# Kernel optimization log

Hardware: AMD Instinct MI355X
Metric: run time of the kernel (lower is better)

The kernel has to match this reference:

```python
import jax, jax.numpy as jnp
import numpy as np

N = 100000; E = 1600000; D_IN = 9; HID = 16; HEADS = 8; D = HID * HEADS; G = 1000
NEG_SLOPE = 0.2; LN_EPS = 1e-5


def _gat_conv(x, src, dst, W, a_src, a_dst, b, heads, ch):
    # PyG GATConv (eval mode, self-loops already appended to src/dst)
    h = (x @ W).reshape(-1, heads, ch)                   # [N,H,C]
    al_s = (h * a_src).sum(-1)                           # [N,H]
    al_d = (h * a_dst).sum(-1)                           # [N,H]
    e = al_s[src] + al_d[dst]                            # [Et,H]
    e = jnp.where(e > 0, e, NEG_SLOPE * e)               # LeakyReLU(0.2)
    m = jax.ops.segment_max(e, dst, num_segments=N)      # per-dst softmax
    alpha = jnp.exp(e - m[dst])
    denom = jax.ops.segment_sum(alpha, dst, num_segments=N)
    alpha = alpha / (denom[dst] + 1e-16)
    out = jax.ops.segment_sum(h[src] * alpha[:, :, None], dst, num_segments=N)
    return out.reshape(-1, heads * ch) + b


def _ln_graph(x, g, b):
    # PyG LayerNorm, mode='graph', batch=None: normalize over all nodes+channels
    mu = x.mean()
    var = jnp.mean((x - mu) ** 2)
    return (x - mu) / jnp.sqrt(var + LN_EPS) * g + b


def setup_inputs() -> dict:
    key = jax.random.key(0)
    ks = jax.random.split(key, 20)
    s = 0.1
    p = lambda i, shape: jax.random.normal(ks[i], shape, jnp.float32) * s
    return {
        "x": jax.random.normal(ks[0], (N, D_IN), jnp.float32),
        "edge_index": jax.random.randint(ks[1], (2, E), 0, N),
        "batch": jnp.sort(jax.random.randint(ks[2], (N,), 0, G)),
        "W1": p(3, (D_IN, D)), "a_src1": p(4, (HEADS, HID)), "a_dst1": p(5, (HEADS, HID)), "b1": jnp.zeros((D,), jnp.float32),
        "W2": p(6, (D, D)), "a_src2": p(7, (1, D)), "a_dst2": p(8, (1, D)), "b2": jnp.zeros((D,), jnp.float32),
        "fc1_w": p(9, (D, D)), "fc1_b": jnp.zeros((D,), jnp.float32),
        "fc2_w": p(10, (D, D)), "fc2_b": jnp.zeros((D,), jnp.float32),
        "fc3_w": p(11, (D, D)), "fc3_b": jnp.zeros((D,), jnp.float32),
        "fc4_w": p(12, (D, D)), "fc4_b": jnp.zeros((D,), jnp.float32),
        "g1": jnp.ones((D,), jnp.float32), "beta1": jnp.zeros((D,), jnp.float32),
        "g2": jnp.ones((D,), jnp.float32), "beta2": jnp.zeros((D,), jnp.float32),
        "fcf_w": p(13, (D, 1)), "fcf_b": jnp.zeros((1,), jnp.float32),
    }


def reference(x, edge_index, batch, W1, a_src1, a_dst1, b1, W2, a_src2, a_dst2, b2,
              fc1_w, fc1_b, fc2_w, fc2_b, fc3_w, fc3_b, fc4_w, fc4_b,
              g1, beta1, g2, beta2, fcf_w, fcf_b):
    loops = jnp.arange(N)
    src = jnp.concatenate([edge_index[0], loops])
    dst = jnp.concatenate([edge_index[1], loops])
    h = jax.nn.relu(_gat_conv(x, src, dst, W1, a_src1, a_dst1, b1, HEADS, HID))
    hc = h
    h = jax.nn.relu(h @ fc1_w + fc1_b)
    h = jax.nn.relu(h @ fc2_w + fc2_b + hc)
    h = _ln_graph(h, g1, beta1)
    hc = h
    h = _gat_conv(h, src, dst, W2, a_src2, a_dst2, b2, 1, D)
    h = jax.nn.relu(h @ fc3_w + fc3_b)
    h = h @ fc4_w + fc4_b + hc
    h = _ln_graph(h, g2, beta2)
    h = h @ fcf_w + fcf_b                                # [N,1]
    sums = jax.ops.segment_sum(h, batch, num_segments=G)
    cnt = jax.ops.segment_sum(jnp.ones((N,), h.dtype), batch, num_segments=G)
    return sums / jnp.maximum(cnt, 1.0)[:, None]          # global_mean_pool -> [G,1]
```

## Files before the change

### kernel.cpp

```cpp
#include <hip/hip_runtime.h>
#include <cstdint>

#define NN 100000
#define NE 1600000
#define DI 9
#define DD 128
#define NH 8
#define NG 1000

#define NBK 3125
#define NBLK 256
#define EPB (NE/NBLK)

typedef unsigned int uint;
typedef __attribute__((ext_vector_type(8))) short bf16x8;
typedef __attribute__((ext_vector_type(4))) float f32x4;

__device__ __forceinline__ float leaky(float x){ return x > 0.f ? x : 0.2f*x; }
__device__ __forceinline__ uint f2bf(float f){
  uint u = __float_as_uint(f);
  return (u + 0x7fffu + ((u>>16)&1u)) >> 16;
}
__device__ __forceinline__ float bflo(uint p){ return __uint_as_float(p << 16); }
__device__ __forceinline__ float bfhi(uint p){ return __uint_as_float(p & 0xffff0000u); }
__device__ __forceinline__ uint packbf(float a, float b){ return f2bf(a) | (f2bf(b)<<16); }

union U16 { uint4 u; bf16x8 v; };
__device__ __forceinline__ bf16x8 ld8(const uint* p){ U16 t; t.u = *(const uint4*)p; return t.v; }

__global__ __launch_bounds__(512) void k_hist(const int* __restrict__ dst, int* __restrict__ hist){
  __shared__ int h[NBK];
  for (int i = threadIdx.x; i < NBK; i += 512) h[i] = 0;
  __syncthreads();
  int blk = blockIdx.x;
  int beg = blk*EPB, end = beg + EPB;
  for (int i = beg + threadIdx.x; i < end; i += 512)
    atomicAdd(&h[dst[i] >> 5], 1);
  __syncthreads();
  for (int b = threadIdx.x; b < NBK; b += 512) hist[b*NBLK + blk] = h[b];
}

__global__ __launch_bounds__(256) void k_bsum(int* __restrict__ hist, int* __restrict__ bsum){
  int b = blockIdx.x*256 + threadIdx.x;
  if (b >= NBK) return;
  int run = 0;
  #pragma unroll 4
  for (int k = 0; k < NBLK; ++k){
    int t = hist[b*NBLK + k];
    hist[b*NBLK + k] = run;
    run += t;
  }
  bsum[b] = run;
}

__global__ __launch_bounds__(1024) void k_bscan(const int* __restrict__ bsum, int* __restrict__ bbase){
  __shared__ int sh[1024];
  __shared__ int carry;
  if (threadIdx.x == 0) carry = 0;
  __syncthreads();
  for (int c0 = 0; c0 < NBK; c0 += 1024){
    int i = c0 + threadIdx.x;
    int v = (i < NBK) ? bsum[i] : 0;
    sh[threadIdx.x] = v;
    __syncthreads();
    for (int off = 1; off < 1024; off <<= 1){
      int t = (threadIdx.x >= off) ? sh[threadIdx.x-off] : 0;
      __syncthreads();
      sh[threadIdx.x] += t;
      __syncthreads();
    }
    if (i < NBK) bbase[i] = carry + sh[threadIdx.x] - v;
    __syncthreads();
    if (threadIdx.x == 0) carry += sh[1023];
    __syncthreads();
  }
}

__global__ __launch_bounds__(512) void k_part(const int* __restrict__ src, const int* __restrict__ dst,
    const int* __restrict__ hist, const int* __restrict__ bbase, uint* __restrict__ ebuf){
  __shared__ int cur[NBK];
  int blk = blockIdx.x;
  for (int b = threadIdx.x; b < NBK; b += 512)
    cur[b] = hist[b*NBLK + blk] + bbase[b];
  __syncthreads();
  int beg = blk*EPB, end = beg + EPB;
  for (int i = beg + threadIdx.x; i < end; i += 512){
    int d = dst[i], s = src[i];
    int b = d >> 5;
    int p = atomicAdd(&cur[b], 1);
    ebuf[p] = (uint)s | ((uint)(d & 31) << 26);
  }
}

__global__ __launch_bounds__(64) void k_fin(const uint* __restrict__ ebuf, const int* __restrict__ bbase,
    const int* __restrict__ bsum, int* __restrict__ rowptr, int* __restrict__ col){
  __shared__ int cnt32[32];
  __shared__ int exc[32];
  int b = blockIdx.x;
  int lane = threadIdx.x;
  if (lane < 32) cnt32[lane] = 0;
  __syncthreads();
  int base = bbase[b], n = bsum[b];
  for (int i = lane; i < n; i += 64)
    atomicAdd(&cnt32[ebuf[base+i] >> 26], 1);
  __syncthreads();
  if (lane == 0){
    int run = 0;
    for (int d = 0; d < 32; ++d){
      int t = cnt32[d];
      exc[d] = run;
      rowptr[b*32 + d] = base + run;
      run += t;
    }
  }
  __syncthreads();
  if (lane < 32) cnt32[lane] = exc[lane];
  __syncthreads();
  for (int i = lane; i < n; i += 64){
    uint e = ebuf[base+i];
    int d = e >> 26;
    int r = atomicAdd(&cnt32[d], 1);
    col[base + r] = (int)(e & 0x03ffffffu);
  }
  if (b == 0 && lane == 0) rowptr[NN] = NE;
}

__global__ __launch_bounds__(64) void k_wconv(const float* __restrict__ W, uint* __restrict__ WT){
  int n = blockIdx.x;
  int t = threadIdx.x;
  float w0 = W[(2*t)*DD + n];
  float w1 = W[(2*t+1)*DD + n];
  WT[n*64 + t] = packbf(w0, w1);
}

__global__ __launch_bounds__(128) void k_lin1(const float* __restrict__ x, const float* __restrict__ W1,
    const float* __restrict__ as1, const float* __restrict__ ad1,
    uint* __restrict__ t1b, float* __restrict__ al_s, float* __restrict__ al_d){
  int n = blockIdx.x;
  int c = threadIdx.x;
  const float* xr = x + n*DI;
  float t = 0.f;
  #pragma unroll
  for (int k = 0; k < DI; ++k) t = fmaf(xr[k], W1[k*DD+c], t);
  uint mybf = f2bf(t);
  uint pbf  = (uint)__shfl_xor((int)mybf, 1, 64);
  if (!(c & 1)) t1b[(size_t)n*64 + (c>>1)] = mybf | (pbf<<16);
  float vs = t * as1[c];
  float vd = t * ad1[c];
  #pragma unroll
  for (int m = 8; m >= 1; m >>= 1){ vs += __shfl_xor(vs, m, 16); vd += __shfl_xor(vd, m, 16); }
  if ((c & 15) == 0){
    al_s[n*NH + (c>>4)] = vs;
    al_d[n*NH + (c>>4)] = vd;
  }
}

__global__ __launch_bounds__(256) void k_gat1(const uint* __restrict__ t1b,
    const float* __restrict__ al_s, const float* __restrict__ al_d,
    const int* __restrict__ rowptr, const int* __restrict__ col,
    const float* __restrict__ b1, uint* __restrict__ outb){
  int n = blockIdx.x*4 + (threadIdx.x >> 6);
  if (n >= NN) return;
  uint lane = threadIdx.x & 63;
  uint h = lane >> 3;
  float ald = al_d[(uint)n*NH + h];
  float a0  = __expf(leaky(al_s[(uint)n*NH + h] + ald));
  uint  ps  = t1b[(uint)n*64u + lane];
  float den = a0;
  float s0 = a0*bflo(ps), s1 = a0*bfhi(ps);
  int beg = rowptr[n], end = rowptr[n+1];
  int e = beg;
  for (; e + 8 <= end; e += 8){
    uint c0 = (uint)col[e],   c1 = (uint)col[e+1], c2 = (uint)col[e+2], c3 = (uint)col[e+3];
    uint c4 = (uint)col[e+4], c5 = (uint)col[e+5], c6 = (uint)col[e+6], c7 = (uint)col[e+7];
    float l0 = al_s[c0*8u + h], l1 = al_s[c1*8u + h], l2 = al_s[c2*8u + h], l3 = al_s[c3*8u + h];
    float l4 = al_s[c4*8u + h], l5 = al_s[c5*8u + h], l6 = al_s[c6*8u + h], l7 = al_s[c7*8u + h];
    uint p0 = t1b[c0*64u + lane], p1 = t1b[c1*64u + lane];
    uint p2 = t1b[c2*64u + lane], p3 = t1b[c3*64u + lane];
    uint p4 = t1b[c4*64u + lane], p5 = t1b[c5*64u + lane];
    uint p6 = t1b[c6*64u + lane], p7 = t1b[c7*64u + lane];
    float a0_ = __expf(leaky(l0 + ald)), a1_ = __expf(leaky(l1 + ald));
    float a2_ = __expf(leaky(l2 + ald)), a3_ = __expf(leaky(l3 + ald));
    float a4_ = __expf(leaky(l4 + ald)), a5_ = __expf(leaky(l5 + ald));
    float a6_ = __expf(leaky(l6 + ald)), a7_ = __expf(leaky(l7 + ald));
    den += a0_ + a1_ + a2_ + a3_ + a4_ + a5_ + a6_ + a7_;
    s0 = fmaf(a0_, bflo(p0), s0); s1 = fmaf(a0_, bfhi(p0), s1);
    s0 = fmaf(a1_, bflo(p1), s0); s1 = fmaf(a1_, bfhi(p1), s1);
    s0 = fmaf(a2_, bflo(p2), s0); s1 = fmaf(a2_, bfhi(p2), s1);
    s0 = fmaf(a3_, bflo(p3), s0); s1 = fmaf(a3_, bfhi(p3), s1);
    s0 = fmaf(a4_, bflo(p4), s0); s1 = fmaf(a4_, bfhi(p4), s1);
    s0 = fmaf(a5_, bflo(p5), s0); s1 = fmaf(a5_, bfhi(p5), s1);
    s0 = fmaf(a6_, bflo(p6), s0); s1 = fmaf(a6_, bfhi(p6), s1);
    s0 = fmaf(a7_, bflo(p7), s0); s1 = fmaf(a7_, bfhi(p7), s1);
  }
  for (; e < end; ++e){
    uint c = (uint)col[e];
    float a = __expf(leaky(al_s[c*8u + h] + ald));
    uint p = t1b[c*64u + lane];
    den += a;
    s0 = fmaf(a, bflo(p), s0); s1 = fmaf(a, bfhi(p), s1);
  }
  float inv = 1.f/(den + 1e-16f);
  float2 bb = ((const float2*)b1)[lane];
  outb[(uint)n*64u + lane] = packbf(fmaxf(s0*inv + bb.x, 0.f), fmaxf(s1*inv + bb.y, 0.f));
}

__global__ __launch_bounds__(256) void k_gat2(const uint* __restrict__ t2b,
    const float* __restrict__ al_s, const float* __restrict__ al_d,
    const int* __restrict__ rowptr, const int* __restrict__ col,
    const float* __restrict__ b2, uint* __restrict__ outb){
  int n = blockIdx.x*4 + (threadIdx.x >> 6);
  if (n >= NN) return;
  uint lane = threadIdx.x & 63;
  float ald = al_d[n];
  float a0  = __expf(leaky(al_s[n] + ald));
  uint  ps  = t2b[(uint)n*64u + lane];
  float den = a0;
  float s0 = a0*bflo(ps), s1 = a0*bfhi(ps);
  int beg = rowptr[n], end = rowptr[n+1];
  int e = beg;
  for (; e + 8 <= end; e += 8){
    uint c0 = (uint)col[e],   c1 = (uint)col[e+1], c2 = (uint)col[e+2], c3 = (uint)col[e+3];
    uint c4 = (uint)col[e+4], c5 = (uint)col[e+5], c6 = (uint)col[e+6], c7 = (uint)col[e+7];
    float l0 = al_s[c0], l1 = al_s[c1], l2 = al_s[c2], l3 = al_s[c3];
    float l4 = al_s[c4], l5 = al_s[c5], l6 = al_s[c6], l7 = al_s[c7];
    uint p0 = t2b[c0*64u + lane], p1 = t2b[c1*64u + lane];
    uint p2 = t2b[c2*64u + lane], p3 = t2b[c3*64u + lane];
    uint p4 = t2b[c4*64u + lane], p5 = t2b[c5*64u + lane];
    uint p6 = t2b[c6*64u + lane], p7 = t2b[c7*64u + lane];
    float a0_ = __expf(leaky(l0 + ald)), a1_ = __expf(leaky(l1 + ald));
    float a2_ = __expf(leaky(l2 + ald)), a3_ = __expf(leaky(l3 + ald));
    float a4_ = __expf(leaky(l4 + ald)), a5_ = __expf(leaky(l5 + ald));
    float a6_ = __expf(leaky(l6 + ald)), a7_ = __expf(leaky(l7 + ald));
    den += a0_ + a1_ + a2_ + a3_ + a4_ + a5_ + a6_ + a7_;
    s0 = fmaf(a0_, bflo(p0), s0); s1 = fmaf(a0_, bfhi(p0), s1);
    s0 = fmaf(a1_, bflo(p1), s0); s1 = fmaf(a1_, bfhi(p1), s1);
    s0 = fmaf(a2_, bflo(p2), s0); s1 = fmaf(a2_, bfhi(p2), s1);
    s0 = fmaf(a3_, bflo(p3), s0); s1 = fmaf(a3_, bfhi(p3), s1);
    s0 = fmaf(a4_, bflo(p4), s0); s1 = fmaf(a4_, bfhi(p4), s1);
    s0 = fmaf(a5_, bflo(p5), s0); s1 = fmaf(a5_, bfhi(p5), s1);
    s0 = fmaf(a6_, bflo(p6), s0); s1 = fmaf(a6_, bfhi(p6), s1);
    s0 = fmaf(a7_, bflo(p7), s0); s1 = fmaf(a7_, bfhi(p7), s1);
  }
  for (; e < end; ++e){
    uint c = (uint)col[e];
    float a = __expf(leaky(al_s[c] + ald));
    uint p = t2b[c*64u + lane];
    den += a;
    s0 = fmaf(a, bflo(p), s0); s1 = fmaf(a, bfhi(p), s1);
  }
  float inv = 1.f/(den + 1e-16f);
  float2 bb = ((const float2*)b2)[lane];
  outb[(uint)n*64u + lane] = packbf(s0*inv + bb.x, s1*inv + bb.y);
}

template<bool RELU, bool BIAS, bool RES, bool LNRED, bool AL2>
__global__ __launch_bounds__(256) void k_mfma(const uint* __restrict__ Xb, const uint* __restrict__ WTb,
    const float* __restrict__ bias, const uint* __restrict__ resb, uint* __restrict__ outb,
    float* __restrict__ pbuf, const float* __restrict__ avs, const float* __restrict__ avd,
    float* __restrict__ o_als, float* __restrict__ o_ald, int nrows){
  int lane = threadIdx.x & 63;
  int wid  = threadIdx.x >> 6;
  int m0 = blockIdx.x*128 + wid*32;
  int lr = lane & 15, hi4 = lane >> 4;
  f32x4 acc[2][8];
  #pragma unroll
  for (int a = 0; a < 2; ++a)
    #pragma unroll
    for (int c = 0; c < 8; ++c) acc[a][c] = (f32x4){0.f,0.f,0.f,0.f};
  int ra0 = m0 + lr;      if (ra0 > NN-1) ra0 = NN-1;
  int ra1 = m0 + 16 + lr; if (ra1 > NN-1) ra1 = NN-1;
  #pragma unroll
  for (int kk = 0; kk < 4; ++kk){
    int ko = kk*16 + hi4*4;
    bf16x8 a0 = ld8(Xb + (size_t)ra0*64 + ko);
    bf16x8 a1 = ld8(Xb + (size_t)ra1*64 + ko);
    #pragma unroll
    for (int c = 0; c < 8; ++c){
      bf16x8 b = ld8(WTb + (size_t)(c*16 + lr)*64 + ko);
      acc[0][c] = __builtin_amdgcn_mfma_f32_16x16x32_bf16(a0, b, acc[0][c], 0, 0, 0);
      acc[1][c] = __builtin_amdgcn_mfma_f32_16x16x32_bf16(a1, b, acc[1][c], 0, 0, 0);
    }
  }
  if (AL2){
    #pragma unroll
    for (int rg = 0; rg < 2; ++rg){
      #pragma unroll
      for (int r = 0; r < 4; ++r){
        float vs = 0.f, vd = 0.f;
        #pragma unroll
        for (int c = 0; c < 8; ++c){
          float v = acc[rg][c][r];
          vs = fmaf(v, avs[c*16 + lr], vs);
          vd = fmaf(v, avd[c*16 + lr], vd);
        }
        #pragma unroll
        for (int m = 8; m >= 1; m >>= 1){ vs += __shfl_xor(vs, m, 64); vd += __shfl_xor(vd, m, 64); }
        int row = m0 + rg*16 + hi4*4 + r;
        if (lr == 0 && row < nrows){ o_als[row] = vs; o_ald[row] = vd; }
      }
    }
  }
  bool evn = !(lane & 1);
  int cph = lr >> 1;
  float lns = 0.f, lnss = 0.f;
  #pragma unroll
  for (int rg = 0; rg < 2; ++rg){
    #pragma unroll
    for (int c = 0; c < 8; ++c){
      int cp = c*8 + cph;
      #pragma unroll
      for (int r = 0; r < 4; ++r){
        float v0 = acc[rg][c][r];
        float v1 = __shfl_xor(v0, 1, 64);
        int row = m0 + rg*16 + hi4*4 + r;
        if (evn && row < nrows){
          if (BIAS){ float2 bb = ((const float2*)bias)[cp]; v0 += bb.x; v1 += bb.y; }
          if (RES){ uint rr = resb[(size_t)row*64 + cp]; v0 += bflo(rr); v1 += bfhi(rr); }
          if (RELU){ v0 = fmaxf(v0, 0.f); v1 = fmaxf(v1, 0.f); }
          outb[(size_t)row*64 + cp] = packbf(v0, v1);
          if (LNRED){ lns += v0 + v1; lnss += v0*v0 + v1*v1; }
        }
      }
    }
  }
  if (LNRED){
    #pragma unroll
    for (int m = 32; m >= 1; m >>= 1){ lns += __shfl_xor(lns, m, 64); lnss += __shfl_xor(lnss, m, 64); }
    __shared__ float shred[8];
    if (lane == 0){ shred[wid*2] = lns; shred[wid*2+1] = lnss; }
    __syncthreads();
    if (threadIdx.x == 0){
      float S = 0.f, SS = 0.f;
      for (int w = 0; w < 4; ++w){ S += shred[2*w]; SS += shred[2*w+1]; }
      pbuf[blockIdx.x*2] = S; pbuf[blockIdx.x*2+1] = SS;
    }
  }
}

__global__ __launch_bounds__(256) void k_ln_stats(const float* __restrict__ pbuf, float* __restrict__ stats, int nb){
  float s = 0.f, ss = 0.f;
  for (int i = threadIdx.x; i < nb; i += 256){ s += pbuf[2*i]; ss += pbuf[2*i+1]; }
  #pragma unroll
  for (int m = 32; m >= 1; m >>= 1){ s += __shfl_xor(s, m, 64); ss += __shfl_xor(ss, m, 64); }
  __shared__ float sh[8];
  int wid = threadIdx.x >> 6, lane = threadIdx.x & 63;
  if (lane == 0){ sh[wid*2] = s; sh[wid*2+1] = ss; }
  __syncthreads();
  if (threadIdx.x == 0){
    float S = 0.f, SS = 0.f;
    for (int w = 0; w < 4; ++w){ S += sh[2*w]; SS += sh[2*w+1]; }
    const float inv = 1.f/((float)NN*(float)DD);
    float mu = S*inv;
    float var = SS*inv - mu*mu;
    stats[0] = mu;
    stats[1] = rsqrtf(var + 1e-5f);
  }
}

__global__ __launch_bounds__(256) void k_ln_apply_bf(uint* __restrict__ xb, const float* __restrict__ g,
    const float* __restrict__ be, const float* __restrict__ stats){
  const int n4 = NN*16;
  float mu = stats[0], rs = stats[1];
  uint4* x4 = (uint4*)xb;
  const float2* g2 = (const float2*)g;
  const float2* b2 = (const float2*)be;
  for (int i = blockIdx.x*256 + threadIdx.x; i < n4; i += gridDim.x*256){
    int cb = (i & 15)*4;
    uint4 u = x4[i];
    float2 ga = g2[cb],   gb = g2[cb+1], gc = g2[cb+2], gd = g2[cb+3];
    float2 ba = b2[cb],   bb = b2[cb+1], bc = b2[cb+2], bd = b2[cb+3];
    u.x = packbf((bflo(u.x)-mu)*rs*ga.x + ba.x, (bfhi(u.x)-mu)*rs*ga.y + ba.y);
    u.y = packbf((bflo(u.y)-mu)*rs*gb.x + bb.x, (bfhi(u.y)-mu)*rs*gb.y + bb.y);
    u.z = packbf((bflo(u.z)-mu)*rs*gc.x + bc.x, (bfhi(u.z)-mu)*rs*gc.y + bc.y);
    u.w = packbf((bflo(u.w)-mu)*rs*gd.x + bd.x, (bfhi(u.w)-mu)*rs*gd.y + bd.y);
    x4[i] = u;
  }
}

__global__ __launch_bounds__(256) void k_fdot_ln(const uint* __restrict__ xb, const float* __restrict__ g,
    const float* __restrict__ be, const float* __restrict__ stats,
    const float* __restrict__ fw, const float* __restrict__ fb, float* __restrict__ val){
  int n = blockIdx.x*4 + (threadIdx.x >> 6);
  if (n >= NN) return;
  int lane = threadIdx.x & 63;
  float mu = stats[0], rs = stats[1];
  uint p = xb[(size_t)n*64 + lane];
  float2 gg = ((const float2*)g)[lane];
  float2 bb = ((const float2*)be)[lane];
  float2 ww = ((const float2*)fw)[lane];
  float v = ((bflo(p)-mu)*rs*gg.x + bb.x)*ww.x + ((bfhi(p)-mu)*rs*gg.y + bb.y)*ww.y;
  #pragma unroll
  for (int m = 32; m >= 1; m >>= 1) v += __shfl_xor(v, m, 64);
  if (lane == 0) val[n] = v + fb[0];
}

__global__ __launch_bounds__(64) void k_pool(const float* __restrict__ val, const int* __restrict__ batch,
                                             float* __restrict__ out){
  int g = blockIdx.x;
  int lane = threadIdx.x;
  int lo = 0, hi = NN;
  while (lo < hi){ int mid = (lo+hi)>>1; if (batch[mid] < g) lo = mid+1; else hi = mid; }
  int start = lo;
  hi = NN;
  while (lo < hi){ int mid = (lo+hi)>>1; if (batch[mid] < g+1) lo = mid+1; else hi = mid; }
  int end = lo;
  float s = 0.f;
  for (int i = start + lane; i < end; i += 64) s += val[i];
  #pragma unroll
  for (int m = 32; m >= 1; m >>= 1) s += __shfl_xor(s, m, 64);
  if (lane == 0) out[g] = s / fmaxf((float)(end - start), 1.f);
}

extern "C" void kernel_launch(void* const* d_in, const int* in_sizes, int n_in,
                              void* d_out, int out_size, void* d_ws, size_t ws_size,
                              hipStream_t stream){
  const float* x   = (const float*)d_in[0];
  const int*   ei  = (const int*)d_in[1];
  const int* batch = (const int*)d_in[2];
  const float* W1  = (const float*)d_in[3];
  const float* as1 = (const float*)d_in[4];
  const float* ad1 = (const float*)d_in[5];
  const float* b1  = (const float*)d_in[6];
  const float* W2  = (const float*)d_in[7];
  const float* as2 = (const float*)d_in[8];
  const float* ad2 = (const float*)d_in[9];
  const float* b2  = (const float*)d_in[10];
  const float* fc1w= (const float*)d_in[11];
  const float* fc1b= (const float*)d_in[12];
  const float* fc2w= (const float*)d_in[13];
  const float* fc2b= (const float*)d_in[14];
  const float* fc3w= (const float*)d_in[15];
  const float* fc3b= (const float*)d_in[16];
  const float* fc4w= (const float*)d_in[17];
  const float* fc4b= (const float*)d_in[18];
  const float* g1  = (const float*)d_in[19];
  const float* be1 = (const float*)d_in[20];
  const float* g2  = (const float*)d_in[21];
  const float* be2 = (const float*)d_in[22];
  const float* fcw = (const float*)d_in[23];
  const float* fcb = (const float*)d_in[24];
  float* out = (float*)d_out;
  (void)in_sizes; (void)n_in; (void)out_size; (void)ws_size;

  char* ws = (char*)d_ws;
  size_t off = 0;
  auto alloc = [&](size_t bytes)->void*{
    void* p = ws + off;
    off += (bytes + 255) & ~(size_t)255;
    return p;
  };
  float* A    = (float*)alloc((size_t)NN*DD*4);
  float* B    = (float*)alloc((size_t)NN*DD*4);
  float* C    = (float*)alloc((size_t)NN*DD*4);
  float* als1 = (float*)alloc((size_t)NN*NH*4);
  float* ald1 = (float*)alloc((size_t)NN*NH*4);
  float* als2 = (float*)alloc((size_t)NN*4);
  float* ald2 = (float*)alloc((size_t)NN*4);
  float* escr = (float*)alloc((size_t)NE*4);
  int*   rowptr = (int*)alloc((size_t)(NN+1)*4);
  int*   col    = (int*)alloc((size_t)NE*4);
  int*   bsum   = (int*)alloc((size_t)NBK*4);
  int*   bbase  = (int*)alloc((size_t)NBK*4);
  float* pbuf   = (float*)alloc(1024*2*4);
  float* stats  = (float*)alloc(2*4);
  float* val    = (float*)alloc((size_t)NN*4);
  uint* wt_fc1  = (uint*)alloc((size_t)DD*64*4);
  uint* wt_fc2  = (uint*)alloc((size_t)DD*64*4);
  uint* wt_w2   = (uint*)alloc((size_t)DD*64*4);
  uint* wt_fc3  = (uint*)alloc((size_t)DD*64*4);
  uint* wt_fc4  = (uint*)alloc((size_t)DD*64*4);

  uint*  Ab     = (uint*)A;
  uint*  Bb     = (uint*)B;
  uint*  Cb     = (uint*)C;
  int*   hist   = (int*)A;
  uint*  ebuf   = (uint*)escr;

  const int* esrc = ei;
  const int* edst = ei + NE;

  k_hist <<<NBLK, 512, 0, stream>>>(edst, hist);
  k_bsum <<<(NBK+255)/256, 256, 0, stream>>>(hist, bsum);
  k_bscan<<<1, 1024, 0, stream>>>(bsum, bbase);
  k_part <<<NBLK, 512, 0, stream>>>(esrc, edst, hist, bbase, ebuf);
  k_fin  <<<NBK, 64, 0, stream>>>(ebuf, bbase, bsum, rowptr, col);

  k_wconv<<<DD, 64, 0, stream>>>(fc1w, wt_fc1);
  k_wconv<<<DD, 64, 0, stream>>>(fc2w, wt_fc2);
  k_wconv<<<DD, 64, 0, stream>>>(W2,   wt_w2);
  k_wconv<<<DD, 64, 0, stream>>>(fc3w, wt_fc3);
  k_wconv<<<DD, 64, 0, stream>>>(fc4w, wt_fc4);

  const int WB = (NN + 3)/4;
  const int GB = (NN + 127)/128;

  k_lin1<<<NN, 128, 0, stream>>>(x, W1, as1, ad1, Ab, als1, ald1);
  k_gat1<<<WB, 256, 0, stream>>>(Ab, als1, ald1, rowptr, col, b1, Bb);

  k_mfma<true,  true, false, false, false><<<GB, 256, 0, stream>>>(Bb, wt_fc1, fc1b, nullptr, Ab, nullptr, nullptr, nullptr, nullptr, nullptr, NN);
  k_mfma<true,  true, true,  true,  false><<<GB, 256, 0, stream>>>(Ab, wt_fc2, fc2b, Bb,      Cb, pbuf,    nullptr, nullptr, nullptr, nullptr, NN);

  k_ln_stats<<<1, 256, 0, stream>>>(pbuf, stats, GB);
  k_ln_apply_bf<<<1024, 256, 0, stream>>>(Cb, g1, be1, stats);

  k_mfma<false, false, false, false, true ><<<GB, 256, 0, stream>>>(Cb, wt_w2, nullptr, nullptr, Ab, nullptr, as2, ad2, als2, ald2, NN);
  k_gat2<<<WB, 256, 0, stream>>>(Ab, als2, ald2, rowptr, col, b2, Bb);

  k_mfma<true,  true, false, false, false><<<GB, 256, 0, stream>>>(Bb, wt_fc3, fc3b, nullptr, Ab, nullptr, nullptr, nullptr, nullptr, nullptr, NN);
  k_mfma<false, true, true,  true,  false><<<GB, 256, 0, stream>>>(Ab, wt_fc4, fc4b, Cb,      Bb, pbuf,    nullptr, nullptr, nullptr, nullptr, NN);

  k_ln_stats<<<1, 256, 0, stream>>>(pbuf, stats, GB);
  k_fdot_ln<<<WB, 256, 0, stream>>>(Bb, g2, be2, stats, fcw, fcb, val);
  k_pool<<<NG, 64, 0, stream>>>(val, batch, out);
}
```

Before: 506.6 us.

## Fuse paired MLP GEMMs through LDS, batch weight conversion, transpose histogram layout

Adds k_mfma2, which runs two back-to-back 128x128 bf16 MFMA GEMMs in one kernel. The ReLU'd intermediate stays in shared memory, so it is never written to and reread from global memory. The kernel also applies the residual, the optional ReLU and the LayerNorm partial sums. The five weight-conversion launches become one kernel that picks its matrix from the block index. The bucket histogram is stored block-major, so the per-bucket prefix loop in k_bsum reads memory coalesced across threads. The fused kernel uses more shared memory and registers per block, which may reduce occupancy.

```diff
diff --git a/kernel.cpp b/kernel.cpp
--- a/kernel.cpp
+++ b/kernel.cpp
@@ -27,6 +27,7 @@
 
 union U16 { uint4 u; bf16x8 v; };
 __device__ __forceinline__ bf16x8 ld8(const uint* p){ U16 t; t.u = *(const uint4*)p; return t.v; }
+__device__ __forceinline__ bf16x8 ld8lds(const uint* p){ U16 t; t.u = *(const uint4*)p; return t.v; }
 
 __global__ __launch_bounds__(512) void k_hist(const int* __restrict__ dst, int* __restrict__ hist){
   __shared__ int h[NBK];
@@ -37,17 +38,16 @@
   for (int i = beg + threadIdx.x; i < end; i += 512)
     atomicAdd(&h[dst[i] >> 5], 1);
   __syncthreads();
-  for (int b = threadIdx.x; b < NBK; b += 512) hist[b*NBLK + blk] = h[b];
+  for (int b = threadIdx.x; b < NBK; b += 512) hist[(size_t)blk*NBK + b] = h[b];
 }
 
 __global__ __launch_bounds__(256) void k_bsum(int* __restrict__ hist, int* __restrict__ bsum){
   int b = blockIdx.x*256 + threadIdx.x;
   if (b >= NBK) return;
   int run = 0;
-  #pragma unroll 4
   for (int k = 0; k < NBLK; ++k){
-    int t = hist[b*NBLK + k];
-    hist[b*NBLK + k] = run;
+    int t = hist[(size_t)k*NBK + b];
+    hist[(size_t)k*NBK + b] = run;
     run += t;
   }
   bsum[b] = run;
@@ -81,7 +81,7 @@
   __shared__ int cur[NBK];
   int blk = blockIdx.x;
   for (int b = threadIdx.x; b < NBK; b += 512)
-    cur[b] = hist[b*NBLK + blk] + bbase[b];
+    cur[b] = hist[(size_t)blk*NBK + b] + bbase[b];
   __syncthreads();
   int beg = blk*EPB, end = beg + EPB;
   for (int i = beg + threadIdx.x; i < end; i += 512){
@@ -125,12 +125,18 @@
   if (b == 0 && lane == 0) rowptr[NN] = NE;
 }
 
-__global__ __launch_bounds__(64) void k_wconv(const float* __restrict__ W, uint* __restrict__ WT){
-  int n = blockIdx.x;
+__global__ __launch_bounds__(64) void k_wconv5(const float* __restrict__ w0, const float* __restrict__ w1,
+    const float* __restrict__ w2, const float* __restrict__ w3, const float* __restrict__ w4,
+    uint* __restrict__ o0, uint* __restrict__ o1, uint* __restrict__ o2,
+    uint* __restrict__ o3, uint* __restrict__ o4){
+  int which = blockIdx.x >> 7;
+  int n = blockIdx.x & 127;
   int t = threadIdx.x;
-  float w0 = W[(2*t)*DD + n];
-  float w1 = W[(2*t+1)*DD + n];
-  WT[n*64 + t] = packbf(w0, w1);
+  const float* W = (which==0)?w0:(which==1)?w1:(which==2)?w2:(which==3)?w3:w4;
+  uint* WT = (which==0)?o0:(which==1)?o1:(which==2)?o2:(which==3)?o3:o4;
+  float a = W[(2*t)*DD + n];
+  float b = W[(2*t+1)*DD + n];
+  WT[n*64 + t] = packbf(a, b);
 }
 
 __global__ __launch_bounds__(128) void k_lin1(const float* __restrict__ x, const float* __restrict__ W1,
@@ -338,6 +344,108 @@
   }
 }
 
+template<bool RELU2>
+__global__ __launch_bounds__(256) void k_mfma2(const uint* __restrict__ Xb,
+    const uint* __restrict__ WT1b, const float* __restrict__ bias1,
+    const uint* __restrict__ WT2b, const float* __restrict__ bias2,
+    const uint* __restrict__ resb, uint* __restrict__ outb,
+    float* __restrict__ pbuf, int nrows){
+  __shared__ uint Y1[128][68];
+  int lane = threadIdx.x & 63;
+  int wid  = threadIdx.x >> 6;
+  int m0 = blockIdx.x*128 + wid*32;
+  int lr = lane & 15, hi4 = lane >> 4;
+  bool evn = !(lane & 1);
+  int cph = lr >> 1;
+  f32x4 acc[2][8];
+  #pragma unroll
+  for (int a = 0; a < 2; ++a)
+    #pragma unroll
+    for (int c = 0; c < 8; ++c) acc[a][c] = (f32x4){0.f,0.f,0.f,0.f};
+  int ra0 = m0 + lr;      if (ra0 > NN-1) ra0 = NN-1;
+  int ra1 = m0 + 16 + lr; if (ra1 > NN-1) ra1 = NN-1;
+  #pragma unroll
+  for (int kk = 0; kk < 4; ++kk){
+    int ko = kk*16 + hi4*4;
+    bf16x8 a0 = ld8(Xb + (size_t)ra0*64 + ko);
+    bf16x8 a1 = ld8(Xb + (size_t)ra1*64 + ko);
+    #pragma unroll
+    for (int c = 0; c < 8; ++c){
+      bf16x8 b = ld8(WT1b + (size_t)(c*16 + lr)*64 + ko);
+      acc[0][c] = __builtin_amdgcn_mfma_f32_16x16x32_bf16(a0, b, acc[0][c], 0, 0, 0);
+      acc[1][c] = __builtin_amdgcn_mfma_f32_16x16x32_bf16(a1, b, acc[1][c], 0, 0, 0);
+    }
+  }
+  #pragma unroll
+  for (int rg = 0; rg < 2; ++rg){
+    #pragma unroll
+    for (int c = 0; c < 8; ++c){
+      int cp = c*8 + cph;
+      #pragma unroll
+      for (int r = 0; r < 4; ++r){
+        float v0 = acc[rg][c][r];
+        float v1 = __shfl_xor(v0, 1, 64);
+        if (evn){
+          float2 bb = ((const float2*)bias1)[cp];
+          v0 = fmaxf(v0 + bb.x, 0.f); v1 = fmaxf(v1 + bb.y, 0.f);
+          int lrow = wid*32 + rg*16 + hi4*4 + r;
+          Y1[lrow][cp] = packbf(v0, v1);
+        }
+      }
+    }
+  }
+  __syncthreads();
+  #pragma unroll
+  for (int a = 0; a < 2; ++a)
+    #pragma unroll
+    for (int c = 0; c < 8; ++c) acc[a][c] = (f32x4){0.f,0.f,0.f,0.f};
+  #pragma unroll
+  for (int kk = 0; kk < 4; ++kk){
+    int ko = kk*16 + hi4*4;
+    bf16x8 a0 = ld8lds(&Y1[wid*32 + lr][ko]);
+    bf16x8 a1 = ld8lds(&Y1[wid*32 + 16 + lr][ko]);
+    #pragma unroll
+    for (int c = 0; c < 8; ++c){
+      bf16x8 b = ld8(WT2b + (size_t)(c*16 + lr)*64 + ko);
+      acc[0][c] = __builtin_amdgcn_mfma_f32_16x16x32_bf16(a0, b, acc[0][c], 0, 0, 0);
+      acc[1][c] = __builtin_amdgcn_mfma_f32_16x16x32_bf16(a1, b, acc[1][c], 0, 0, 0);
+    }
+  }
+  float lns = 0.f, lnss = 0.f;
+  #pragma unroll
+  for (int rg = 0; rg < 2; ++rg){
+    #pragma unroll
+    for (int c = 0; c < 8; ++c){
+      int cp = c*8 + cph;
+      #pragma unroll
+      for (int r = 0; r < 4; ++r){
+        float v0 = acc[rg][c][r];
+        float v1 = __shfl_xor(v0, 1, 64);
+        int row = m0 + rg*16 + hi4*4 + r;
+        if (evn && row < nrows){
+          float2 bb = ((const float2*)bias2)[cp];
+          v0 += bb.x; v1 += bb.y;
+          uint rr = resb[(size_t)row*64 + cp];
+          v0 += bflo(rr); v1 += bfhi(rr);
+          if (RELU2){ v0 = fmaxf(v0, 0.f); v1 = fmaxf(v1, 0.f); }
+          outb[(size_t)row*64 + cp] = packbf(v0, v1);
+          lns += v0 + v1; lnss += v0*v0 + v1*v1;
+        }
+      }
+    }
+  }
+  #pragma unroll
+  for (int m = 32; m >= 1; m >>= 1){ lns += __shfl_xor(lns, m, 64); lnss += __shfl_xor(lnss, m, 64); }
+  __shared__ float shred[8];
+  if (lane == 0){ shred[wid*2] = lns; shred[wid*2+1] = lnss; }
+  __syncthreads();
+  if (threadIdx.x == 0){
+    float S = 0.f, SS = 0.f;
+    for (int w = 0; w < 4; ++w){ S += shred[2*w]; SS += shred[2*w+1]; }
+    pbuf[blockIdx.x*2] = S; pbuf[blockIdx.x*2+1] = SS;
+  }
+}
+
 __global__ __launch_bounds__(256) void k_ln_stats(const float* __restrict__ pbuf, float* __restrict__ stats, int nb){
   float s = 0.f, ss = 0.f;
   for (int i = threadIdx.x; i < nb; i += 256){ s += pbuf[2*i]; ss += pbuf[2*i+1]; }
@@ -486,11 +594,8 @@
   k_part <<<NBLK, 512, 0, stream>>>(esrc, edst, hist, bbase, ebuf);
   k_fin  <<<NBK, 64, 0, stream>>>(ebuf, bbase, bsum, rowptr, col);
 
-  k_wconv<<<DD, 64, 0, stream>>>(fc1w, wt_fc1);
-  k_wconv<<<DD, 64, 0, stream>>>(fc2w, wt_fc2);
-  k_wconv<<<DD, 64, 0, stream>>>(W2,   wt_w2);
-  k_wconv<<<DD, 64, 0, stream>>>(fc3w, wt_fc3);
-  k_wconv<<<DD, 64, 0, stream>>>(fc4w, wt_fc4);
+  k_wconv5<<<5*DD, 64, 0, stream>>>(fc1w, fc2w, W2, fc3w, fc4w,
+                                    wt_fc1, wt_fc2, wt_w2, wt_fc3, wt_fc4);
 
   const int WB = (NN + 3)/4;
   const int GB = (NN + 127)/128;
@@ -498,8 +603,7 @@
   k_lin1<<<NN, 128, 0, stream>>>(x, W1, as1, ad1, Ab, als1, ald1);
   k_gat1<<<WB, 256, 0, stream>>>(Ab, als1, ald1, rowptr, col, b1, Bb);
 
-  k_mfma<true,  true, false, false, false><<<GB, 256, 0, stream>>>(Bb, wt_fc1, fc1b, nullptr, Ab, nullptr, nullptr, nullptr, nullptr, nullptr, NN);
-  k_mfma<true,  true, true,  true,  false><<<GB, 256, 0, stream>>>(Ab, wt_fc2, fc2b, Bb,      Cb, pbuf,    nullptr, nullptr, nullptr, nullptr, NN);
+  k_mfma2<true><<<GB, 256, 0, stream>>>(Bb, wt_fc1, fc1b, wt_fc2, fc2b, Bb, Cb, pbuf, NN);
 
   k_ln_stats<<<1, 256, 0, stream>>>(pbuf, stats, GB);
   k_ln_apply_bf<<<1024, 256, 0, stream>>>(Cb, g1, be1, stats);
@@ -507,8 +611,7 @@
   k_mfma<false, false, false, false, true ><<<GB, 256, 0, stream>>>(Cb, wt_w2, nullptr, nullptr, Ab, nullptr, as2, ad2, als2, ald2, NN);
   k_gat2<<<WB, 256, 0, stream>>>(Ab, als2, ald2, rowptr, col, b2, Bb);
 
-  k_mfma<true,  true, false, false, false><<<GB, 256, 0, stream>>>(Bb, wt_fc3, fc3b, nullptr, Ab, nullptr, nullptr, nullptr, nullptr, nullptr, NN);
-  k_mfma<false, true, true,  true,  false><<<GB, 256, 0, stream>>>(Ab, wt_fc4, fc4b, Cb,      Bb, pbuf,    nullptr, nullptr, nullptr, nullptr, NN);
+  k_mfma2<false><<<GB, 256, 0, stream>>>(Bb, wt_fc3, fc3b, wt_fc4, fc4b, Cb, Bb, pbuf, NN);
 
   k_ln_stats<<<1, 256, 0, stream>>>(pbuf, stats, GB);
   k_fdot_ln<<<WB, 256, 0, stream>>>(Bb, g2, be2, stats, fcw, fcb, val);
```

Result: slower. 533.8 us (+5.4%).

## Transpose histogram layout for coalesced scans and fuse weight conversion launches

Applied to the files above, without the earlier changes.

Stores the per-block bucket histogram block-major instead of bucket-major, so the histogram write, the per-bucket prefix loop and the partition read become coalesced across threads. The five separate weight bf16 conversion kernels are merged into a single launch that selects the matrix from the block index. The aim is to cut strided global memory traffic in the CSR build and remove four kernel launch overheads.

```diff
diff --git a/kernel.cpp b/kernel.cpp
--- a/kernel.cpp
+++ b/kernel.cpp
@@ -37,17 +37,16 @@
   for (int i = beg + threadIdx.x; i < end; i += 512)
     atomicAdd(&h[dst[i] >> 5], 1);
   __syncthreads();
-  for (int b = threadIdx.x; b < NBK; b += 512) hist[b*NBLK + blk] = h[b];
+  for (int b = threadIdx.x; b < NBK; b += 512) hist[(size_t)blk*NBK + b] = h[b];
 }
 
 __global__ __launch_bounds__(256) void k_bsum(int* __restrict__ hist, int* __restrict__ bsum){
   int b = blockIdx.x*256 + threadIdx.x;
   if (b >= NBK) return;
   int run = 0;
-  #pragma unroll 4
   for (int k = 0; k < NBLK; ++k){
-    int t = hist[b*NBLK + k];
-    hist[b*NBLK + k] = run;
+    int t = hist[(size_t)k*NBK + b];
+    hist[(size_t)k*NBK + b] = run;
     run += t;
   }
   bsum[b] = run;
@@ -81,7 +80,7 @@
   __shared__ int cur[NBK];
   int blk = blockIdx.x;
   for (int b = threadIdx.x; b < NBK; b += 512)
-    cur[b] = hist[b*NBLK + blk] + bbase[b];
+    cur[b] = hist[(size_t)blk*NBK + b] + bbase[b];
   __syncthreads();
   int beg = blk*EPB, end = beg + EPB;
   for (int i = beg + threadIdx.x; i < end; i += 512){
@@ -125,12 +124,18 @@
   if (b == 0 && lane == 0) rowptr[NN] = NE;
 }
 
-__global__ __launch_bounds__(64) void k_wconv(const float* __restrict__ W, uint* __restrict__ WT){
-  int n = blockIdx.x;
+__global__ __launch_bounds__(64) void k_wconv5(const float* __restrict__ w0, const float* __restrict__ w1,
+    const float* __restrict__ w2, const float* __restrict__ w3, const float* __restrict__ w4,
+    uint* __restrict__ o0, uint* __restrict__ o1, uint* __restrict__ o2,
+    uint* __restrict__ o3, uint* __restrict__ o4){
+  int which = blockIdx.x >> 7;
+  int n = blockIdx.x & 127;
   int t = threadIdx.x;
-  float w0 = W[(2*t)*DD + n];
-  float w1 = W[(2*t+1)*DD + n];
-  WT[n*64 + t] = packbf(w0, w1);
+  const float* W = (which==0)?w0:(which==1)?w1:(which==2)?w2:(which==3)?w3:w4;
+  uint* WT = (which==0)?o0:(which==1)?o1:(which==2)?o2:(which==3)?o3:o4;
+  float a = W[(2*t)*DD + n];
+  float b = W[(2*t+1)*DD + n];
+  WT[n*64 + t] = packbf(a, b);
 }
 
 __global__ __launch_bounds__(128) void k_lin1(const float* __restrict__ x, const float* __restrict__ W1,
@@ -486,11 +491,8 @@
   k_part <<<NBLK, 512, 0, stream>>>(esrc, edst, hist, bbase, ebuf);
   k_fin  <<<NBK, 64, 0, stream>>>(ebuf, bbase, bsum, rowptr, col);
 
-  k_wconv<<<DD, 64, 0, stream>>>(fc1w, wt_fc1);
-  k_wconv<<<DD, 64, 0, stream>>>(fc2w, wt_fc2);
-  k_wconv<<<DD, 64, 0, stream>>>(W2,   wt_w2);
-  k_wconv<<<DD, 64, 0, stream>>>(fc3w, wt_fc3);
-  k_wconv<<<DD, 64, 0, stream>>>(fc4w, wt_fc4);
+  k_wconv5<<<5*DD, 64, 0, stream>>>(fc1w, fc2w, W2, fc3w, fc4w,
+                                    wt_fc1, wt_fc2, wt_w2, wt_fc3, wt_fc4);
 
   const int WB = (NN + 3)/4;
   const int GB = (NN + 127)/128;
```

Measured after the change: 481.1 us. -5.0%, faster.
